# Performance work log

Measured on AMD Instinct MI355X. Metric: run time of the kernel, lower is better.

Reference implementation:

```python
import jax, jax.numpy as jnp
import numpy as np
import math

BLOCK = 256
NUM_HEADS = 32
HEAD_DIM = 128
HIDDEN = 2048
INNER = NUM_HEADS * HEAD_DIM
SEQ = 4096
EPS = 1e-5
LAYER_IDX = 0
NUM_LAYERS = 32


def _build_slopes(n):
    def get_slopes(n):
        def pow2(m):
            start = 2 ** (-2 ** (-(math.log2(m) - 3)))
            return [start * start ** i for i in range(m)]
        if math.log2(n).is_integer():
            return pow2(n)
        c = 2 ** math.floor(math.log2(n))
        return pow2(c) + get_slopes(2 * c)[0::2][: n - c]
    s = np.asarray(get_slopes(n), dtype=np.float32).reshape(n, 1, 1)
    # layer decay scaling as in __init__
    s = s * (1.0 - LAYER_IDX / (NUM_LAYERS - 1) + 1e-5)
    return s


def setup_inputs() -> dict:
    key = jax.random.key(0)
    k1, k2, k3, k4 = jax.random.split(key, 4)
    sd_h = 1.0 / math.sqrt(HIDDEN)
    sd_i = 1.0 / math.sqrt(INNER)
    return {
        "hidden_states": jax.random.normal(k1, (SEQ, HIDDEN), jnp.float32),
        "w_qkv": jax.random.normal(k2, (HIDDEN, 3 * INNER), jnp.float32) * sd_h,
        "w_gate": jax.random.normal(k3, (HIDDEN, INNER), jnp.float32) * sd_h,
        "w_out": jax.random.normal(k4, (INNER, HIDDEN), jnp.float32) * sd_i,
        "norm_weight": jnp.ones((INNER,), jnp.float32),
        "slope_rate": jnp.asarray(_build_slopes(NUM_HEADS)),
        "kv_cache": jnp.zeros((NUM_HEADS, HEAD_DIM, HEAD_DIM), jnp.float32),
    }


def _lightning_attention(q, k, v, slope, kv0):
    # q,k,v: [h, n, d]; slope: [h,1,1]; kv0: [h, d, d]
    h, n, d = q.shape
    nb = n // BLOCK
    qb = q.reshape(h, nb, BLOCK, d).transpose(1, 0, 2, 3)  # [nb,h,B,d]
    kb = k.reshape(h, nb, BLOCK, d).transpose(1, 0, 2, 3)
    vb = v.reshape(h, nb, BLOCK, d).transpose(1, 0, 2, 3)

    idx = jnp.arange(BLOCK, dtype=jnp.float32)
    diff = idx[:, None] - idx[None, :]                      # i - j
    s = slope.reshape(h, 1, 1)
    intra_decay = jnp.where(diff >= 0, jnp.exp(-s * diff), 0.0)   # [h,B,B]
    q_decay = jnp.exp(-s * (idx + 1.0).reshape(1, BLOCK, 1))      # [h,B,1]
    k_decay = jnp.exp(-s * (BLOCK - 1.0 - idx).reshape(1, BLOCK, 1))  # [h,B,1]
    block_decay = jnp.exp(-s * BLOCK)                             # [h,1,1]

    def step(kv, blk):
        qc, kc, vc = blk  # each [h,B,d]
        scores = jnp.einsum('hid,hjd->hij', qc, kc) * intra_decay
        o_intra = jnp.einsum('hij,hjd->hid', scores, vc)
        o_inter = q_decay * jnp.einsum('hid,hde->hie', qc, kv)
        kv_new = block_decay * kv + jnp.einsum('hjd,hje->hde', kc * k_decay, vc)
        return kv_new, o_intra + o_inter

    kv_final, outs = jax.lax.scan(step, kv0, (qb, kb, vb))
    out = outs.transpose(1, 0, 2, 3).reshape(h, n, d)
    return out, kv_final


def reference(hidden_states, w_qkv, w_gate, w_out, norm_weight, slope_rate, kv_cache):
    n = hidden_states.shape[0]
    # qkv projection + SiLU activation (done in fp32 in the original)
    qkv = jax.nn.silu(hidden_states @ w_qkv)                  # [n, 3*inner]
    qkv = qkv.reshape(n, NUM_HEADS, 3 * HEAD_DIM)
    q, k, v = jnp.split(qkv, 3, axis=-1)                      # [n,h,d] each
    q = q.transpose(1, 0, 2)                                  # [h,n,d]
    k = k.transpose(1, 0, 2)
    v = v.transpose(1, 0, 2)

    attn, kv_final = _lightning_attention(q, k, v, slope_rate, kv_cache)
    attn = attn.transpose(1, 0, 2).reshape(n, INNER)          # n (h d)

    # RMSNorm (fp32) then sigmoid gate then output projection
    var = jnp.mean(attn * attn, axis=-1, keepdims=True)
    normed = attn * jax.lax.rsqrt(var + EPS) * norm_weight
    gate = jax.nn.sigmoid(hidden_states @ w_gate)
    out = (gate * normed) @ w_out                             # [n, hidden]
    return out
```

## Files before the change

### kernel.cpp

```cpp
#include <hip/hip_runtime.h>
#include <stdint.h>

typedef __bf16 bf16x8 __attribute__((ext_vector_type(8)));
typedef float  f32x4  __attribute__((ext_vector_type(4)));
typedef unsigned short u16x8 __attribute__((ext_vector_type(8)));

__device__ __forceinline__ unsigned short f2bf(float f) {
    union { float f; uint32_t u; } x; x.f = f;
    uint32_t r = (x.u + 0x7FFFu + ((x.u >> 16) & 1u)) >> 16;
    return (unsigned short)r;
}
__device__ __forceinline__ float bf2f(unsigned short b) {
    union { uint32_t u; float f; } x; x.u = ((uint32_t)b) << 16;
    return x.f;
}

__device__ __forceinline__ void gl16(const void* g, void* l) {
    __builtin_amdgcn_global_load_lds(
        (const __attribute__((address_space(1))) void*)g,
        (__attribute__((address_space(3))) void*)(uint32_t)(uintptr_t)l,
        16, 0, 0);
}

#define MFMA16(a, b, c) __builtin_amdgcn_mfma_f32_16x16x32_bf16((a), (b), (c), 0, 0, 0)

__global__ __launch_bounds__(256) void f32_to_bf16_kernel(const float* __restrict__ in,
                                                          unsigned short* __restrict__ out,
                                                          int n8) {
    int i = blockIdx.x * 256 + threadIdx.x;
    if (i >= n8) return;
    float4 a = ((const float4*)in)[2 * i];
    float4 b = ((const float4*)in)[2 * i + 1];
    u16x8 o;
    o[0] = f2bf(a.x); o[1] = f2bf(a.y); o[2] = f2bf(a.z); o[3] = f2bf(a.w);
    o[4] = f2bf(b.x); o[5] = f2bf(b.y); o[6] = f2bf(b.z); o[7] = f2bf(b.w);
    ((u16x8*)out)[i] = o;
}

__global__ __launch_bounds__(256) void transpose_w_kernel(const float* __restrict__ in,
                                                          unsigned short* __restrict__ out,
                                                          int R, int C) {
    __shared__ float tile[32][33];
    int c0 = blockIdx.x * 32, r0 = blockIdx.y * 32;
    int lx = threadIdx.x & 31, ly = threadIdx.x >> 5;
#pragma unroll
    for (int i = ly; i < 32; i += 8)
        tile[i][lx] = in[(size_t)(r0 + i) * C + c0 + lx];
    __syncthreads();
#pragma unroll
    for (int i = ly; i < 32; i += 8)
        out[(size_t)(c0 + i) * R + r0 + lx] = f2bf(tile[lx][i]);
}

template <int ACT, int OUTF32>
__global__ __launch_bounds__(512, 2) void gemm256_kernel(const unsigned short* __restrict__ A,
                                                         const unsigned short* __restrict__ Bt,
                                                         void* __restrict__ Cout,
                                                         int N, int K, int NBN) {
    __shared__ unsigned short Abuf[2][2][8192];
    __shared__ unsigned short Bbuf[2][2][8192];

    int bid = blockIdx.x;
    int xcd = bid & 7, kw = bid >> 3;
    int bm = (xcd & 3) * 4 + (kw & 3);
    int bn = (xcd >> 2) * (NBN >> 1) + (kw >> 2);
    int tid = threadIdx.x, lane = tid & 63, w = tid >> 6;
    int wr = w >> 2, wc = w & 3;

    int r0 = tid >> 3;
    int cbs = (tid & 7) << 4;
    int el0 = (cbs ^ ((r0 & 7) << 4)) >> 1;
    int r1 = 64 + r0;
    int el1 = (cbs ^ ((r1 & 7) << 4)) >> 1;
    int lo0 = tid * 16, lo1 = 8192 + tid * 16;

    const unsigned short* Ag0 = A + (size_t)(bm * 256) * K;
    const unsigned short* Ag1 = A + (size_t)(bm * 256 + 128) * K;
    const unsigned short* Bg0 = Bt + (size_t)(bn * 256) * K;
    const unsigned short* Bg1 = Bt + (size_t)(bn * 256 + 128) * K;

#define STAGE(src, dstHalf, k0)                                            \
    do {                                                                   \
        gl16((src) + (size_t)r0 * K + (k0) + el0, (char*)(dstHalf) + lo0); \
        gl16((src) + (size_t)r1 * K + (k0) + el1, (char*)(dstHalf) + lo1); \
    } while (0)

    int aRow = wr * 64 + (lane & 15);
    int bRow = wc * 32 + (lane & 15);
    int swz = (lane & 7) << 4;
    int cbb = (lane >> 4) << 4;

#define RD_A(slot, R, m, kk) \
    af[R][m][kk] = *(const bf16x8*)((const char*)Abuf[slot][R] + ((aRow + (m) * 16) << 7) + (((kk) * 64 + cbb) ^ swz))
#define RD_B(slot, Cq, n, kk) \
    bfr[Cq][n][kk] = *(const bf16x8*)((const char*)Bbuf[slot][Cq] + ((bRow + (n) * 16) << 7) + (((kk) * 64 + cbb) ^ swz))

#define QUAD(q, Rh, Cc)                                                       \
    do {                                                                      \
        _Pragma("unroll")                                                     \
        for (int m = 0; m < 4; ++m)                                           \
            _Pragma("unroll")                                                 \
            for (int n = 0; n < 2; ++n) {                                     \
                acc[q][m][n] = MFMA16(af[Rh][m][0], bfr[Cc][n][0], acc[q][m][n]); \
                acc[q][m][n] = MFMA16(af[Rh][m][1], bfr[Cc][n][1], acc[q][m][n]); \
            }                                                                 \
    } while (0)

    bf16x8 af[2][4][2];
    bf16x8 bfr[2][2][2];
    f32x4 acc[4][4][2];
#pragma unroll
    for (int q = 0; q < 4; ++q)
#pragma unroll
        for (int m = 0; m < 4; ++m)
#pragma unroll
            for (int n = 0; n < 2; ++n)
#pragma unroll
                for (int r = 0; r < 4; ++r) acc[q][m][n][r] = 0.f;

    int NT = K >> 6;
    STAGE(Ag0, Abuf[0][0], 0);
    STAGE(Bg0, Bbuf[0][0], 0);
    STAGE(Ag1, Abuf[0][1], 0);
    STAGE(Bg1, Bbuf[0][1], 0);
    STAGE(Ag0, Abuf[1][0], 64);
    STAGE(Bg0, Bbuf[1][0], 64);
    STAGE(Ag1, Abuf[1][1], 64);
    STAGE(Bg1, Bbuf[1][1], 64);
    asm volatile("s_waitcnt vmcnt(8)" ::: "memory");
    __builtin_amdgcn_s_barrier();
#pragma unroll
    for (int m = 0; m < 4; ++m) { RD_A(0, 0, m, 0); RD_A(0, 0, m, 1); }
#pragma unroll
    for (int n = 0; n < 2; ++n) { RD_B(0, 0, n, 0); RD_B(0, 0, n, 1); }

    for (int t = 0; t < NT; ++t) {
        int cur = t & 1, nx = cur ^ 1;
        bool rd = (t + 1 < NT);
        bool st = (t + 2 < NT);
        int ks = (t + 2) << 6;

#pragma unroll
        for (int m = 0; m < 4; ++m) { RD_A(cur, 1, m, 0); RD_A(cur, 1, m, 1); }
        asm volatile("s_waitcnt lgkmcnt(8)" ::: "memory");
        __builtin_amdgcn_sched_barrier(0);
        __builtin_amdgcn_s_setprio(1);
        QUAD(0, 0, 0);
        __builtin_amdgcn_s_setprio(0);

#pragma unroll
        for (int n = 0; n < 2; ++n) { RD_B(cur, 1, n, 0); RD_B(cur, 1, n, 1); }
        asm volatile("s_waitcnt lgkmcnt(4)" ::: "memory");
        __builtin_amdgcn_sched_barrier(0);
        __builtin_amdgcn_s_setprio(1);
        QUAD(1, 1, 0);
        __builtin_amdgcn_s_setprio(0);

        asm volatile("s_waitcnt lgkmcnt(0)" ::: "memory");
        asm volatile("s_waitcnt vmcnt(0)" ::: "memory");
        __builtin_amdgcn_s_barrier();
        if (st) {
            STAGE(Ag0, Abuf[cur][0], ks);
            STAGE(Bg0, Bbuf[cur][0], ks);
        }
        if (rd) {
#pragma unroll
            for (int n = 0; n < 2; ++n) { RD_B(nx, 0, n, 0); RD_B(nx, 0, n, 1); }
        }
        __builtin_amdgcn_s_setprio(1);
        QUAD(2, 0, 1);
        __builtin_amdgcn_s_setprio(0);

        if (st) {
            STAGE(Ag1, Abuf[cur][1], ks);
            STAGE(Bg1, Bbuf[cur][1], ks);
        }
        if (rd) {
#pragma unroll
            for (int m = 0; m < 4; ++m) { RD_A(nx, 0, m, 0); RD_A(nx, 0, m, 1); }
        }
        __builtin_amdgcn_s_setprio(1);
        QUAD(3, 1, 1);
        __builtin_amdgcn_s_setprio(0);
    }

#pragma unroll
    for (int q = 0; q < 4; ++q) {
        const int R_ = q & 1, C_ = q >> 1;
#pragma unroll
        for (int m = 0; m < 4; ++m) {
            int row0 = bm * 256 + R_ * 128 + wr * 64 + m * 16 + ((lane >> 4) * 4);
#pragma unroll
            for (int n = 0; n < 2; ++n) {
                int col = bn * 256 + C_ * 128 + wc * 32 + n * 16 + (lane & 15);
#pragma unroll
                for (int rg = 0; rg < 4; ++rg) {
                    float v = acc[q][m][n][rg];
                    if (ACT == 1) v = v / (1.f + __expf(-v));
                    else if (ACT == 2) v = 1.f / (1.f + __expf(-v));
                    size_t idx = (size_t)(row0 + rg) * N + col;
                    if (OUTF32) ((float*)Cout)[idx] = v;
                    else        ((unsigned short*)Cout)[idx] = f2bf(v);
                }
            }
        }
    }
#undef STAGE
#undef RD_A
#undef RD_B
#undef QUAD
}

template <int ACT, int OUTBF>
__global__ __launch_bounds__(256) void gemm_bt_kernel(const unsigned short* __restrict__ A,
                                                      const unsigned short* __restrict__ Bt,
                                                      void* __restrict__ Cp,
                                                      int M, int N, int K) {
    __shared__ unsigned short As[128 * 64];
    __shared__ unsigned short Bs[128 * 64];
    int bn = blockIdx.x, bm = blockIdx.y;
    int tid = threadIdx.x, lane = tid & 63, w = tid >> 6;
    int wr = w >> 1, wc = w & 1;

    f32x4 acc[4][4];
#pragma unroll
    for (int m = 0; m < 4; ++m)
#pragma unroll
        for (int n = 0; n < 4; ++n)
#pragma unroll
            for (int r = 0; r < 4; ++r) acc[m][n][r] = 0.f;

    const size_t Abase = (size_t)bm * 128 * K;
    const size_t Bbase = (size_t)bn * 128 * K;

    for (int k0 = 0; k0 < K; k0 += 64) {
        __syncthreads();
#pragma unroll
        for (int it = 0; it < 4; ++it) {
            int slot = it * 256 + tid;
            int o = slot * 16;
            int r = o >> 7;
            int cb = o & 127;
            int scb = cb ^ ((r & 7) << 4);
            gl16(A + Abase + (size_t)r * K + k0 + (scb >> 1), (char*)As + o);
            gl16(Bt + Bbase + (size_t)r * K + k0 + (scb >> 1), (char*)Bs + o);
        }
        __syncthreads();
#pragma unroll
        for (int kk = 0; kk < 2; ++kk) {
            int kb = kk * 64 + ((lane >> 4) * 16);
            bf16x8 af[4], bfr[4];
#pragma unroll
            for (int m = 0; m < 4; ++m) {
                int r = wr * 64 + m * 16 + (lane & 15);
                af[m] = *(const bf16x8*)((const char*)As + (r << 7) + (kb ^ ((r & 7) << 4)));
            }
#pragma unroll
            for (int n = 0; n < 4; ++n) {
                int r = wc * 64 + n * 16 + (lane & 15);
                bfr[n] = *(const bf16x8*)((const char*)Bs + (r << 7) + (kb ^ ((r & 7) << 4)));
            }
#pragma unroll
            for (int m = 0; m < 4; ++m)
#pragma unroll
                for (int n = 0; n < 4; ++n)
                    acc[m][n] = MFMA16(af[m], bfr[n], acc[m][n]);
        }
    }

#pragma unroll
    for (int m = 0; m < 4; ++m) {
        int rowb = bm * 128 + wr * 64 + m * 16 + ((lane >> 4) * 4);
#pragma unroll
        for (int n = 0; n < 4; ++n) {
            int col = bn * 128 + wc * 64 + n * 16 + (lane & 15);
#pragma unroll
            for (int r = 0; r < 4; ++r) {
                float v = acc[m][n][r];
                if (ACT == 1) v = v / (1.f + __expf(-v));
                else if (ACT == 2) v = 1.f / (1.f + __expf(-v));
                size_t idx = (size_t)(rowb + r) * N + col;
                if (OUTBF) ((unsigned short*)Cp)[idx] = f2bf(v);
                else       ((float*)Cp)[idx] = v;
            }
        }
    }
}

__global__ __launch_bounds__(256) void kv_transpose_kernel(const unsigned short* __restrict__ qkv,
                                                           const float* __restrict__ slopes,
                                                           unsigned short* __restrict__ kts,
                                                           unsigned short* __restrict__ vt) {
    __shared__ unsigned short tk[32][33];
    __shared__ unsigned short tv[32][33];
    int n0 = blockIdx.x * 32, d0 = blockIdx.y * 32, h = blockIdx.z;
    float s = slopes[h];
    int lx = threadIdx.x & 31, ly = threadIdx.x >> 5;
#pragma unroll
    for (int i = ly; i < 32; i += 8) {
        int n = n0 + i;
        size_t rowb = (size_t)n * 12288 + h * 384;
        float kv = bf2f(qkv[rowb + 128 + d0 + lx]) * __expf(-s * (float)(255 - (n & 255)));
        tk[i][lx] = f2bf(kv);
        tv[i][lx] = qkv[rowb + 256 + d0 + lx];
    }
    __syncthreads();
#pragma unroll
    for (int i = ly; i < 32; i += 8) {
        size_t ob = (size_t)(h * 128 + d0 + i) * 4096 + n0 + lx;
        kts[ob] = tk[lx][i];
        vt[ob] = tv[lx][i];
    }
}

__global__ __launch_bounds__(256) void kv_outer_kernel(const unsigned short* __restrict__ kts,
                                                       const unsigned short* __restrict__ vt,
                                                       float* __restrict__ U) {
    __shared__ unsigned short Kc[128 * 64];
    __shared__ unsigned short Vc[128 * 64];
    int blk = blockIdx.x;
    int h = blk & 31, t = blk >> 5;
    int tid = threadIdx.x, lane = tid & 63, w = tid >> 6;

    f32x4 acc[2][8];
#pragma unroll
    for (int m = 0; m < 2; ++m)
#pragma unroll
        for (int n = 0; n < 8; ++n)
#pragma unroll
            for (int r = 0; r < 4; ++r) acc[m][n][r] = 0.f;

    for (int ks = 0; ks < 4; ++ks) {
        __syncthreads();
#pragma unroll
        for (int it = 0; it < 4; ++it) {
            int slot = it * 256 + tid;
            int o = slot * 16;
            int r = o >> 7;
            int cb = o & 127;
            int scb = cb ^ ((r & 7) << 4);
            size_t j = (size_t)t * 256 + ks * 64 + (scb >> 1);
            gl16(kts + (size_t)(h * 128 + r) * 4096 + j, (char*)Kc + o);
            gl16(vt + (size_t)(h * 128 + r) * 4096 + j, (char*)Vc + o);
        }
        __syncthreads();
#pragma unroll
        for (int kk = 0; kk < 2; ++kk) {
            int kb = kk * 64 + ((lane >> 4) * 16);
            bf16x8 vf[2], kf[8];
#pragma unroll
            for (int m = 0; m < 2; ++m) {
                int e = w * 32 + m * 16 + (lane & 15);
                vf[m] = *(const bf16x8*)((const char*)Vc + (e << 7) + (kb ^ ((e & 7) << 4)));
            }
#pragma unroll
            for (int n = 0; n < 8; ++n) {
                int d = n * 16 + (lane & 15);
                kf[n] = *(const bf16x8*)((const char*)Kc + (d << 7) + (kb ^ ((d & 7) << 4)));
            }
#pragma unroll
            for (int m = 0; m < 2; ++m)
#pragma unroll
                for (int n = 0; n < 8; ++n)
                    acc[m][n] = MFMA16(vf[m], kf[n], acc[m][n]);
        }
    }
    size_t base = (size_t)(h * 16 + t) * 16384;
#pragma unroll
    for (int m = 0; m < 2; ++m)
#pragma unroll
        for (int n = 0; n < 8; ++n)
#pragma unroll
            for (int r = 0; r < 4; ++r) {
                int e = w * 32 + m * 16 + ((lane >> 4) * 4) + r;
                int d = n * 16 + (lane & 15);
                U[base + (size_t)e * 128 + d] = acc[m][n][r];
            }
}

__global__ __launch_bounds__(256) void kv_scan_kernel(const float* __restrict__ kv_cache,
                                                      const float* __restrict__ U,
                                                      const float* __restrict__ slopes,
                                                      unsigned short* __restrict__ Wb) {
    __shared__ float Tt[16][132];
    int h = blockIdx.x >> 3;
    int c = blockIdx.x & 7;
    int c0 = c * 2048, e0 = c * 16;
    int tid = threadIdx.x;
    float s = slopes[h];
    float bd = __expf(-s * 256.f);
    size_t hb = (size_t)h * 16384;
#pragma unroll
    for (int it = 0; it < 8; ++it) {
        int d = it * 16 + (tid >> 4);
        Tt[tid & 15][d] = kv_cache[hb + (size_t)d * 128 + e0 + (tid & 15)];
    }
    __syncthreads();
    float wst[8];
#pragma unroll
    for (int i = 0; i < 8; ++i) {
        int e_rel = i * 2 + (tid >> 7);
        wst[i] = Tt[e_rel][tid & 127];
    }
    for (int t = 0; t < 16; ++t) {
        size_t base = (size_t)(h * 16 + t) * 16384 + c0;
#pragma unroll
        for (int i = 0; i < 8; ++i) {
            int idx = i * 256 + tid;
            Wb[base + idx] = f2bf(wst[i]);
            wst[i] = bd * wst[i] + U[base + idx];
        }
    }
}

__global__ __launch_bounds__(256, 2) void attn_out_kernel(const unsigned short* __restrict__ qkv,
                                                          const unsigned short* __restrict__ vt,
                                                          const unsigned short* __restrict__ Wb,
                                                          const float* __restrict__ slopes,
                                                          unsigned short* __restrict__ attn) {
    __shared__ unsigned short lds[40960];
    unsigned short* Qs = lds;
    unsigned short* Ps = lds + 16384;
    unsigned short* KW = lds + 24576;
    unsigned short* Ks = KW;
    unsigned short* Vs = KW + 8192;

    int blk = blockIdx.x;
    int h = blk & 31, tq = blk >> 5;
    int t = tq >> 1, qh = tq & 1;
    float s = slopes[h];
    int tid = threadIdx.x, lane = tid & 63, w = tid >> 6;
    int rowbase = t * 256 + qh * 128;

#pragma unroll
    for (int it = 0; it < 8; ++it) {
        int o = (it * 256 + tid) * 16;
        int r = o >> 8, cb = o & 255, scb = cb ^ ((r & 7) << 4);
        gl16(qkv + (size_t)(rowbase + r) * 12288 + h * 384 + (scb >> 1), (char*)Qs + o);
    }
#pragma unroll
    for (int it = 0; it < 8; ++it) {
        int o = (it * 256 + tid) * 16;
        int e = o >> 8, cb = o & 255, scb = cb ^ ((e & 7) << 4);
        gl16(Wb + (size_t)((h * 16 + t) * 128 + e) * 128 + (scb >> 1), (char*)KW + o);
    }
    __syncthreads();

    f32x4 acc[2][8];
#pragma unroll
    for (int m = 0; m < 2; ++m)
#pragma unroll
        for (int n = 0; n < 8; ++n)
#pragma unroll
            for (int r = 0; r < 4; ++r) acc[m][n][r] = 0.f;

#pragma unroll
    for (int kk = 0; kk < 4; ++kk) {
        int kb = kk * 64 + ((lane >> 4) * 16);
        bf16x8 qf[2], wf[8];
#pragma unroll
        for (int m = 0; m < 2; ++m) {
            int r = w * 32 + m * 16 + (lane & 15);
            qf[m] = *(const bf16x8*)((const char*)Qs + (r << 8) + (kb ^ ((r & 7) << 4)));
        }
#pragma unroll
        for (int n = 0; n < 8; ++n) {
            int e = n * 16 + (lane & 15);
            wf[n] = *(const bf16x8*)((const char*)KW + (e << 8) + (kb ^ ((e & 7) << 4)));
        }
#pragma unroll
        for (int m = 0; m < 2; ++m)
#pragma unroll
            for (int n = 0; n < 8; ++n)
                acc[m][n] = MFMA16(qf[m], wf[n], acc[m][n]);
    }
#pragma unroll
    for (int m = 0; m < 2; ++m)
#pragma unroll
        for (int rg = 0; rg < 4; ++rg) {
            int i = qh * 128 + w * 32 + m * 16 + ((lane >> 4) * 4) + rg;
            float qd = __expf(-s * (float)(i + 1));
#pragma unroll
            for (int n = 0; n < 8; ++n) acc[m][n][rg] *= qd;
        }

    int jbmax = ((qh << 2) + w) >> 1;
    for (int jb = 0; jb < 4; ++jb) {
        __syncthreads();
#pragma unroll
        for (int it = 0; it < 4; ++it) {
            int o = (it * 256 + tid) * 16;
            int r = o >> 8, cb = o & 255, scb = cb ^ ((r & 7) << 4);
            gl16(qkv + (size_t)(t * 256 + jb * 64 + r) * 12288 + h * 384 + 128 + (scb >> 1),
                 (char*)Ks + o);
        }
#pragma unroll
        for (int it = 0; it < 4; ++it) {
            int o = (it * 256 + tid) * 16;
            int e = o >> 7, cb = o & 127, scb = cb ^ ((e & 7) << 4);
            gl16(vt + (size_t)(h * 128 + e) * 4096 + t * 256 + jb * 64 + (scb >> 1),
                 (char*)Vs + o);
        }
        __syncthreads();

        if (jb <= jbmax) {
            f32x4 sc[2][4];
#pragma unroll
            for (int m = 0; m < 2; ++m)
#pragma unroll
                for (int n = 0; n < 4; ++n)
#pragma unroll
                    for (int r = 0; r < 4; ++r) sc[m][n][r] = 0.f;
#pragma unroll
            for (int kk = 0; kk < 4; ++kk) {
                int kb = kk * 64 + ((lane >> 4) * 16);
                bf16x8 qf[2], kf[4];
#pragma unroll
                for (int m = 0; m < 2; ++m) {
                    int r = w * 32 + m * 16 + (lane & 15);
                    qf[m] = *(const bf16x8*)((const char*)Qs + (r << 8) + (kb ^ ((r & 7) << 4)));
                }
#pragma unroll
                for (int n = 0; n < 4; ++n) {
                    int r = n * 16 + (lane & 15);
                    kf[n] = *(const bf16x8*)((const char*)Ks + (r << 8) + (kb ^ ((r & 7) << 4)));
                }
#pragma unroll
                for (int m = 0; m < 2; ++m)
#pragma unroll
                    for (int n = 0; n < 4; ++n)
                        sc[m][n] = MFMA16(qf[m], kf[n], sc[m][n]);
            }
            unsigned short* Pw = Ps + w * 2048;
#pragma unroll
            for (int m = 0; m < 2; ++m)
#pragma unroll
                for (int n = 0; n < 4; ++n)
#pragma unroll
                    for (int rg = 0; rg < 4; ++rg) {
                        int il = m * 16 + ((lane >> 4) * 4) + rg;
                        int i = qh * 128 + w * 32 + il;
                        int jl = n * 16 + (lane & 15);
                        int j = jb * 64 + jl;
                        float v = 0.f;
                        if (i >= j) v = sc[m][n][rg] * __expf(-s * (float)(i - j));
                        int cb2 = (jl * 2) ^ ((il & 7) << 4);
                        *(unsigned short*)((char*)Pw + (il << 7) + cb2) = f2bf(v);
                    }
            asm volatile("s_waitcnt lgkmcnt(0)" ::: "memory");
#pragma unroll
            for (int kk = 0; kk < 2; ++kk) {
                int kb = kk * 64 + ((lane >> 4) * 16);
                bf16x8 pf[2], vf[8];
#pragma unroll
                for (int m = 0; m < 2; ++m) {
                    int il = m * 16 + (lane & 15);
                    pf[m] = *(const bf16x8*)((const char*)Pw + (il << 7) + (kb ^ ((il & 7) << 4)));
                }
#pragma unroll
                for (int n = 0; n < 8; ++n) {
                    int e = n * 16 + (lane & 15);
                    vf[n] = *(const bf16x8*)((const char*)Vs + (e << 7) + (kb ^ ((e & 7) << 4)));
                }
#pragma unroll
                for (int m = 0; m < 2; ++m)
#pragma unroll
                    for (int n = 0; n < 8; ++n)
                        acc[m][n] = MFMA16(pf[m], vf[n], acc[m][n]);
            }
        }
    }

#pragma unroll
    for (int m = 0; m < 2; ++m)
#pragma unroll
        for (int n = 0; n < 8; ++n)
#pragma unroll
            for (int rg = 0; rg < 4; ++rg) {
                int i = qh * 128 + w * 32 + m * 16 + ((lane >> 4) * 4) + rg;
                int col = h * 128 + n * 16 + (lane & 15);
                attn[(size_t)(t * 256 + i) * 4096 + col] = f2bf(acc[m][n][rg]);
            }
}

__global__ __launch_bounds__(256) void rms_gate_kernel(const unsigned short* __restrict__ attn,
                                                       const unsigned short* __restrict__ gate,
                                                       const float* __restrict__ nw,
                                                       unsigned short* __restrict__ gated) {
    int row = blockIdx.x, tid = threadIdx.x;
    int lane = tid & 63, w = tid >> 6;
    const unsigned short* ar = attn + (size_t)row * 4096 + tid * 16;
    u16x8 a0 = *(const u16x8*)ar;
    u16x8 a1 = *(const u16x8*)(ar + 8);
    float v[16];
    float ss = 0.f;
#pragma unroll
    for (int j = 0; j < 8; ++j) { v[j] = bf2f(a0[j]); v[8 + j] = bf2f(a1[j]); }
#pragma unroll
    for (int j = 0; j < 16; ++j) ss += v[j] * v[j];
#pragma unroll
    for (int o = 32; o > 0; o >>= 1) ss += __shfl_xor(ss, o);
    __shared__ float red[4];
    if (lane == 0) red[w] = ss;
    __syncthreads();
    float tot = red[0] + red[1] + red[2] + red[3];
    float rs = rsqrtf(tot * (1.f / 4096.f) + 1e-5f);
    const unsigned short* gr = gate + (size_t)row * 4096 + tid * 16;
    u16x8 g0 = *(const u16x8*)gr;
    u16x8 g1 = *(const u16x8*)(gr + 8);
    const float* nwp = nw + tid * 16;
    u16x8 o0, o1;
#pragma unroll
    for (int j = 0; j < 8; ++j) {
        o0[j] = f2bf(v[j] * rs * nwp[j] * bf2f(g0[j]));
        o1[j] = f2bf(v[8 + j] * rs * nwp[8 + j] * bf2f(g1[j]));
    }
    unsigned short* gp = gated + (size_t)row * 4096 + tid * 16;
    *(u16x8*)gp = o0;
    *(u16x8*)(gp + 8) = o1;
}

extern "C" void kernel_launch(void* const* d_in, const int* in_sizes, int n_in,
                              void* d_out, int out_size, void* d_ws, size_t ws_size,
                              hipStream_t stream) {
    const float* hs       = (const float*)d_in[0];
    const float* w_qkv    = (const float*)d_in[1];
    const float* w_gate   = (const float*)d_in[2];
    const float* w_out    = (const float*)d_in[3];
    const float* nw       = (const float*)d_in[4];
    const float* slopes   = (const float*)d_in[5];
    const float* kv_cache = (const float*)d_in[6];
    float* out = (float*)d_out;
    char* ws = (char*)d_ws;

    unsigned short* hsb  = (unsigned short*)(ws + 0);
    unsigned short* wqt  = (unsigned short*)(ws + 16777216);
    unsigned short* wgt  = (unsigned short*)(ws + 67108864);
    unsigned short* wot  = (unsigned short*)(ws + 83886080);
    unsigned short* qkv  = (unsigned short*)(ws + 100663296);
    unsigned short* gate = (unsigned short*)(ws + 201326592);
    unsigned short* kts  = (unsigned short*)(ws + 234881024);
    unsigned short* vt   = (unsigned short*)(ws + 268435456);
    float*          U    = (float*)(ws + 301989888);
    unsigned short* Wb   = (unsigned short*)(ws + 335544320);
    unsigned short* attn  = wqt;
    unsigned short* gated = qkv;

    f32_to_bf16_kernel<<<4096, 256, 0, stream>>>(hs, hsb, 1048576);
    {
        dim3 g(384, 64);
        transpose_w_kernel<<<g, 256, 0, stream>>>(w_qkv, wqt, 2048, 12288);
    }
    {
        dim3 g(128, 64);
        transpose_w_kernel<<<g, 256, 0, stream>>>(w_gate, wgt, 2048, 4096);
    }
    {
        dim3 g(64, 128);
        transpose_w_kernel<<<g, 256, 0, stream>>>(w_out, wot, 4096, 2048);
    }
    gemm256_kernel<1, 0><<<768, 512, 0, stream>>>(hsb, wqt, qkv, 12288, 2048, 48);
    gemm256_kernel<2, 0><<<256, 512, 0, stream>>>(hsb, wgt, gate, 4096, 2048, 16);
    {
        dim3 g(128, 4, 32);
        kv_transpose_kernel<<<g, 256, 0, stream>>>(qkv, slopes, kts, vt);
    }
    kv_outer_kernel<<<512, 256, 0, stream>>>(kts, vt, U);
    kv_scan_kernel<<<256, 256, 0, stream>>>(kv_cache, U, slopes, Wb);
    attn_out_kernel<<<1024, 256, 0, stream>>>(qkv, vt, Wb, slopes, attn);
    rms_gate_kernel<<<4096, 256, 0, stream>>>(attn, gate, nw, gated);
    {
        dim3 g(16, 32);
        gemm_bt_kernel<0, 0><<<g, 256, 0, stream>>>(gated, wot, out, 4096, 2048, 4096);
    }
}
```

Before: 539.2 us.

## Restructure GEMM main loop into per-quarter staged global loads with finer barriers

```diff
diff --git a/kernel.cpp b/kernel.cpp
--- a/kernel.cpp
+++ b/kernel.cpp
@@ -23,6 +23,8 @@
 }
 
 #define MFMA16(a, b, c) __builtin_amdgcn_mfma_f32_16x16x32_bf16((a), (b), (c), 0, 0, 0)
+#define SBAR()  do { __builtin_amdgcn_s_barrier(); __builtin_amdgcn_sched_barrier(0); } while (0)
+#define LGKM0() do { asm volatile("s_waitcnt lgkmcnt(0)" ::: "memory"); __builtin_amdgcn_sched_barrier(0); } while (0)
 
 __global__ __launch_bounds__(256) void f32_to_bf16_kernel(const float* __restrict__ in,
                                                           unsigned short* __restrict__ out,
@@ -90,10 +92,10 @@
     int swz = (lane & 7) << 4;
     int cbb = (lane >> 4) << 4;
 
-#define RD_A(slot, R, m, kk) \
-    af[R][m][kk] = *(const bf16x8*)((const char*)Abuf[slot][R] + ((aRow + (m) * 16) << 7) + (((kk) * 64 + cbb) ^ swz))
-#define RD_B(slot, Cq, n, kk) \
-    bfr[Cq][n][kk] = *(const bf16x8*)((const char*)Bbuf[slot][Cq] + ((bRow + (n) * 16) << 7) + (((kk) * 64 + cbb) ^ swz))
+#define RD_A(d, R, m, kk) \
+    af[R][m][kk] = *(const bf16x8*)((const char*)Abuf[d][R] + ((aRow + (m) * 16) << 7) + (((kk) * 64 + cbb) ^ swz))
+#define RD_B(d, Cq, n, kk) \
+    bfr[Cq][n][kk] = *(const bf16x8*)((const char*)Bbuf[d][Cq] + ((bRow + (n) * 16) << 7) + (((kk) * 64 + cbb) ^ swz))
 
 #define QUAD(q, Rh, Cc)                                                       \
     do {                                                                      \
@@ -124,64 +126,61 @@
     STAGE(Ag1, Abuf[0][1], 0);
     STAGE(Bg1, Bbuf[0][1], 0);
     STAGE(Ag0, Abuf[1][0], 64);
-    STAGE(Bg0, Bbuf[1][0], 64);
-    STAGE(Ag1, Abuf[1][1], 64);
-    STAGE(Bg1, Bbuf[1][1], 64);
-    asm volatile("s_waitcnt vmcnt(8)" ::: "memory");
-    __builtin_amdgcn_s_barrier();
-#pragma unroll
-    for (int m = 0; m < 4; ++m) { RD_A(0, 0, m, 0); RD_A(0, 0, m, 1); }
-#pragma unroll
-    for (int n = 0; n < 2; ++n) { RD_B(0, 0, n, 0); RD_B(0, 0, n, 1); }
+    asm volatile("s_waitcnt vmcnt(6)" ::: "memory");
+    SBAR();
 
     for (int t = 0; t < NT; ++t) {
-        int cur = t & 1, nx = cur ^ 1;
-        bool rd = (t + 1 < NT);
-        bool st = (t + 2 < NT);
-        int ks = (t + 2) << 6;
-
-#pragma unroll
-        for (int m = 0; m < 4; ++m) { RD_A(cur, 1, m, 0); RD_A(cur, 1, m, 1); }
-        asm volatile("s_waitcnt lgkmcnt(8)" ::: "memory");
-        __builtin_amdgcn_sched_barrier(0);
+        int d = t & 1, nx = d ^ 1;
+        bool sA = (t + 1 < NT);
+        int kn = (t + 1) << 6;
+
+#pragma unroll
+        for (int m = 0; m < 4; ++m) { RD_A(d, 0, m, 0); RD_A(d, 0, m, 1); }
+#pragma unroll
+        for (int n = 0; n < 2; ++n) { RD_B(d, 0, n, 0); RD_B(d, 0, n, 1); }
+        if (sA) {
+            STAGE(Bg0, Bbuf[nx][0], kn);
+            asm volatile("s_waitcnt vmcnt(6)" ::: "memory");
+        } else {
+            asm volatile("s_waitcnt vmcnt(2)" ::: "memory");
+        }
+        SBAR();
+        LGKM0();
         __builtin_amdgcn_s_setprio(1);
         QUAD(0, 0, 0);
         __builtin_amdgcn_s_setprio(0);
 
 #pragma unroll
-        for (int n = 0; n < 2; ++n) { RD_B(cur, 1, n, 0); RD_B(cur, 1, n, 1); }
-        asm volatile("s_waitcnt lgkmcnt(4)" ::: "memory");
-        __builtin_amdgcn_sched_barrier(0);
+        for (int m = 0; m < 4; ++m) { RD_A(d, 1, m, 0); RD_A(d, 1, m, 1); }
+        if (sA) {
+            STAGE(Ag1, Abuf[nx][1], kn);
+            asm volatile("s_waitcnt vmcnt(6)" ::: "memory");
+        } else {
+            asm volatile("s_waitcnt vmcnt(0)" ::: "memory");
+        }
+        SBAR();
+        LGKM0();
         __builtin_amdgcn_s_setprio(1);
         QUAD(1, 1, 0);
         __builtin_amdgcn_s_setprio(0);
 
-        asm volatile("s_waitcnt lgkmcnt(0)" ::: "memory");
-        asm volatile("s_waitcnt vmcnt(0)" ::: "memory");
-        __builtin_amdgcn_s_barrier();
-        if (st) {
-            STAGE(Ag0, Abuf[cur][0], ks);
-            STAGE(Bg0, Bbuf[cur][0], ks);
-        }
-        if (rd) {
-#pragma unroll
-            for (int n = 0; n < 2; ++n) { RD_B(nx, 0, n, 0); RD_B(nx, 0, n, 1); }
-        }
+#pragma unroll
+        for (int n = 0; n < 2; ++n) { RD_B(d, 1, n, 0); RD_B(d, 1, n, 1); }
+        if (sA) STAGE(Bg1, Bbuf[nx][1], kn);
+        LGKM0();
         __builtin_amdgcn_s_setprio(1);
         QUAD(2, 0, 1);
         __builtin_amdgcn_s_setprio(0);
 
-        if (st) {
-            STAGE(Ag1, Abuf[cur][1], ks);
-            STAGE(Bg1, Bbuf[cur][1], ks);
-        }
-        if (rd) {
-#pragma unroll
-            for (int m = 0; m < 4; ++m) { RD_A(nx, 0, m, 0); RD_A(nx, 0, m, 1); }
-        }
+        if (t + 2 < NT) STAGE(Ag0, Abuf[d][0], (t + 2) << 6);
         __builtin_amdgcn_s_setprio(1);
         QUAD(3, 1, 1);
         __builtin_amdgcn_s_setprio(0);
+        if (sA) {
+            if (t + 2 < NT) asm volatile("s_waitcnt vmcnt(6)" ::: "memory");
+            else            asm volatile("s_waitcnt vmcnt(4)" ::: "memory");
+            SBAR();
+        }
     }
 
 #pragma unroll
```

Result: no change. 543.7 us (+0.8%).

## Merge QKV and gate GEMMs into one launch and widen weight transpose tiles

Applied to the files above, without the earlier changes.

```diff
diff --git a/kernel.cpp b/kernel.cpp
--- a/kernel.cpp
+++ b/kernel.cpp
@@ -40,23 +40,36 @@
 __global__ __launch_bounds__(256) void transpose_w_kernel(const float* __restrict__ in,
                                                           unsigned short* __restrict__ out,
                                                           int R, int C) {
-    __shared__ float tile[32][33];
-    int c0 = blockIdx.x * 32, r0 = blockIdx.y * 32;
-    int lx = threadIdx.x & 31, ly = threadIdx.x >> 5;
-#pragma unroll
-    for (int i = ly; i < 32; i += 8)
-        tile[i][lx] = in[(size_t)(r0 + i) * C + c0 + lx];
+    __shared__ float tile[64][65];
+    int c0 = blockIdx.x * 64, r0 = blockIdx.y * 64;
+    int tid = threadIdx.x;
+    int tr = tid >> 4;
+    int tc4 = (tid & 15) * 4;
+#pragma unroll
+    for (int it = 0; it < 4; ++it) {
+        int r = it * 16 + tr;
+        float4 v = *(const float4*)&in[(size_t)(r0 + r) * C + c0 + tc4];
+        tile[r][tc4] = v.x; tile[r][tc4 + 1] = v.y;
+        tile[r][tc4 + 2] = v.z; tile[r][tc4 + 3] = v.w;
+    }
     __syncthreads();
 #pragma unroll
-    for (int i = ly; i < 32; i += 8)
-        out[(size_t)(c0 + i) * R + r0 + lx] = f2bf(tile[lx][i]);
-}
-
-template <int ACT, int OUTF32>
-__global__ __launch_bounds__(512, 2) void gemm256_kernel(const unsigned short* __restrict__ A,
-                                                         const unsigned short* __restrict__ Bt,
-                                                         void* __restrict__ Cout,
-                                                         int N, int K, int NBN) {
+    for (int it = 0; it < 4; ++it) {
+        int c = it * 16 + tr;
+        ushort4 o;
+        o.x = f2bf(tile[tc4][c]);
+        o.y = f2bf(tile[tc4 + 1][c]);
+        o.z = f2bf(tile[tc4 + 2][c]);
+        o.w = f2bf(tile[tc4 + 3][c]);
+        *(ushort4*)&out[(size_t)(c0 + c) * R + r0 + tc4] = o;
+    }
+}
+
+__global__ __launch_bounds__(512, 2) void gemm_qkvgate_kernel(const unsigned short* __restrict__ A,
+                                                              const unsigned short* __restrict__ Bt,
+                                                              unsigned short* __restrict__ qkvp,
+                                                              unsigned short* __restrict__ gatep,
+                                                              int K, int NBN, int NQ) {
     __shared__ unsigned short Abuf[2][2][8192];
     __shared__ unsigned short Bbuf[2][2][8192];
 
@@ -184,6 +197,10 @@
         __builtin_amdgcn_s_setprio(0);
     }
 
+    bool isQ = (bn < NQ);
+    unsigned short* outp = isQ ? qkvp : gatep;
+    int Nout = isQ ? 12288 : 4096;
+    int colb0 = (isQ ? bn : bn - NQ) * 256;
 #pragma unroll
     for (int q = 0; q < 4; ++q) {
         const int R_ = q & 1, C_ = q >> 1;
@@ -192,15 +209,13 @@
             int row0 = bm * 256 + R_ * 128 + wr * 64 + m * 16 + ((lane >> 4) * 4);
 #pragma unroll
             for (int n = 0; n < 2; ++n) {
-                int col = bn * 256 + C_ * 128 + wc * 32 + n * 16 + (lane & 15);
+                int col = colb0 + C_ * 128 + wc * 32 + n * 16 + (lane & 15);
 #pragma unroll
                 for (int rg = 0; rg < 4; ++rg) {
                     float v = acc[q][m][n][rg];
-                    if (ACT == 1) v = v / (1.f + __expf(-v));
-                    else if (ACT == 2) v = 1.f / (1.f + __expf(-v));
-                    size_t idx = (size_t)(row0 + rg) * N + col;
-                    if (OUTF32) ((float*)Cout)[idx] = v;
-                    else        ((unsigned short*)Cout)[idx] = f2bf(v);
+                    float sig = 1.f / (1.f + __expf(-v));
+                    float r = isQ ? v * sig : sig;
+                    outp[(size_t)(row0 + rg) * Nout + col] = f2bf(r);
                 }
             }
         }
@@ -648,19 +663,18 @@
 
     f32_to_bf16_kernel<<<4096, 256, 0, stream>>>(hs, hsb, 1048576);
     {
-        dim3 g(384, 64);
+        dim3 g(192, 32);
         transpose_w_kernel<<<g, 256, 0, stream>>>(w_qkv, wqt, 2048, 12288);
     }
     {
-        dim3 g(128, 64);
+        dim3 g(64, 32);
         transpose_w_kernel<<<g, 256, 0, stream>>>(w_gate, wgt, 2048, 4096);
     }
     {
-        dim3 g(64, 128);
+        dim3 g(32, 64);
         transpose_w_kernel<<<g, 256, 0, stream>>>(w_out, wot, 4096, 2048);
     }
-    gemm256_kernel<1, 0><<<768, 512, 0, stream>>>(hsb, wqt, qkv, 12288, 2048, 48);
-    gemm256_kernel<2, 0><<<256, 512, 0, stream>>>(hsb, wgt, gate, 4096, 2048, 16);
+    gemm_qkvgate_kernel<<<1024, 512, 0, stream>>>(hsb, wqt, qkv, gate, 2048, 64, 48);
     {
         dim3 g(128, 4, 32);
         kv_transpose_kernel<<<g, 256, 0, stream>>>(qkv, slopes, kts, vt);
```

New measurement: 507.5 us. -5.9%, faster.
